# Performance work log

Measured on AMD Instinct MI355X. Metric: run time of the kernel, lower is better.

The kernel has to match this reference:

```python
import jax, jax.numpy as jnp
import numpy as np

N = 100000   # nodes
E = 600000   # edges
V = 64       # vocab
D = 128      # emb_dim
H = 128      # hidden_dim
G = 256      # graphs in batch


def setup_inputs():
    key = jax.random.key(0)
    ks = jax.random.split(key, 12)
    x_idx = jax.random.randint(ks[0], (N,), 0, V)
    edge_index = jax.random.randint(ks[1], (2, E), 0, N)
    batch = jnp.sort(jax.random.randint(ks[2], (N,), 0, G))
    emb = jax.random.normal(ks[3], (V, D), jnp.float32) * 0.02
    emb = emb.at[0].set(0.0)  # padding_idx=0
    def lin(k, o, i):
        return jax.random.normal(k, (o, i), jnp.float32) * (1.0 / np.sqrt(i))
    return dict(
        x_idx=x_idx, edge_index=edge_index, batch=batch, emb=emb,
        ln0_g=jnp.ones((D,), jnp.float32), ln0_b=jnp.zeros((D,), jnp.float32),
        w0_l=lin(ks[4], H, D), b0_l=jnp.zeros((H,), jnp.float32), w0_r=lin(ks[5], H, D),
        ln1_g=jnp.ones((H,), jnp.float32), ln1_b=jnp.zeros((H,), jnp.float32),
        w1_l=lin(ks[6], H, H), b1_l=jnp.zeros((H,), jnp.float32), w1_r=lin(ks[7], H, H),
        mlp_w1=lin(ks[8], H // 2, H), mlp_b1=jnp.zeros((H // 2,), jnp.float32),
        mlp_w2=lin(ks[9], 2, H // 2), mlp_b2=jnp.zeros((2,), jnp.float32),
    )


def _layernorm(x, g, b, eps=1e-5):
    m = jnp.mean(x, axis=-1, keepdims=True)
    v = jnp.var(x, axis=-1, keepdims=True)
    return (x - m) * jax.lax.rsqrt(v + eps) * g + b


def _sage_conv(x, src, dst, w_l, b_l, w_r):
    # PyG SAGEConv (mean aggr): out = lin_l(mean_{j->i} x_j) + lin_r(x_i)
    agg = jax.ops.segment_sum(x[src], dst, num_segments=N)        # [N, F]
    deg = jax.ops.segment_sum(jnp.ones((src.shape[0],), x.dtype), dst, num_segments=N)
    agg = agg / jnp.maximum(deg, 1.0)[:, None]
    return agg @ w_l.T + b_l + x @ w_r.T


def reference(x_idx, edge_index, batch, emb,
              ln0_g, ln0_b, w0_l, b0_l, w0_r,
              ln1_g, ln1_b, w1_l, b1_l, w1_r,
              mlp_w1, mlp_b1, mlp_w2, mlp_b2):
    src, dst = edge_index[0], edge_index[1]
    x = emb[x_idx]                                   # [N, D]
    # layer 0 (dropout is identity in eval mode)
    x = _layernorm(x, ln0_g, ln0_b)
    x = jax.nn.relu(_sage_conv(x, src, dst, w0_l, b0_l, w0_r))
    # layer 1
    x = _layernorm(x, ln1_g, ln1_b)
    x = jax.nn.relu(_sage_conv(x, src, dst, w1_l, b1_l, w1_r))
    # global mean pool over graphs
    sums = jax.ops.segment_sum(x, batch, num_segments=G)          # [G, H]
    cnts = jax.ops.segment_sum(jnp.ones((N,), x.dtype), batch, num_segments=G)
    g = sums / jnp.maximum(cnts, 1.0)[:, None]
    # MLP head
    h = jax.nn.relu(g @ mlp_w1.T + mlp_b1)
    return h @ mlp_w2.T + mlp_b2                                   # [G, 2]
```

## Files before the change

kernel.cpp:

```cpp
#include <hip/hip_runtime.h>

#define NN 100000
#define NE 600000
#define DIM 128
#define NG 256
#define NGRP 6250
#define NB_SCAN 391

typedef __attribute__((ext_vector_type(8))) short short8_t;
typedef __attribute__((ext_vector_type(4))) float f32x4;

__device__ __forceinline__ ushort f2bf(float f) {
  unsigned u = __float_as_uint(f);
  unsigned r = (u + 0x7fffu + ((u >> 16) & 1u)) >> 16;
  return (ushort)r;
}
__device__ __forceinline__ float bf2f(ushort h) {
  return __uint_as_float(((unsigned)h) << 16);
}

__global__ __launch_bounds__(256) void embed_ln_kernel(
    const int* __restrict__ x_idx, const float* __restrict__ emb,
    const float* __restrict__ g, const float* __restrict__ b,
    float* __restrict__ out) {
  int wave = threadIdx.x >> 6;
  int lane = threadIdx.x & 63;
  int n = blockIdx.x * 4 + wave;
  if (n >= NN) return;
  int idx = x_idx[n];
  float2 v = ((const float2*)(emb + (size_t)idx * DIM))[lane];
  float s = v.x + v.y;
  float sq = v.x * v.x + v.y * v.y;
  for (int off = 32; off; off >>= 1) {
    s += __shfl_xor(s, off);
    sq += __shfl_xor(sq, off);
  }
  float m = s * (1.0f / 128.0f);
  float var = sq * (1.0f / 128.0f) - m * m;
  float r = rsqrtf(var + 1e-5f);
  float2 gg = ((const float2*)g)[lane];
  float2 bb = ((const float2*)b)[lane];
  float2 o;
  o.x = (v.x - m) * r * gg.x + bb.x;
  o.y = (v.y - m) * r * gg.y + bb.y;
  ((float2*)(out + (size_t)n * DIM))[lane] = o;
}

__global__ __launch_bounds__(256) void deg_int_kernel(const int* __restrict__ dst,
                                                      int* __restrict__ degi) {
  int e = blockIdx.x * 256 + threadIdx.x;
  if (e < NE) atomicAdd(degi + dst[e], 1);
}

__global__ __launch_bounds__(256) void scan1_kernel(const int* __restrict__ degi,
                                                    int* __restrict__ excl,
                                                    int* __restrict__ bsum) {
  __shared__ int tmp[256];
  int t = threadIdx.x;
  int i = blockIdx.x * 256 + t;
  int v = (i < NN) ? degi[i] : 0;
  int val = v;
  tmp[t] = val;
  __syncthreads();
  for (int off = 1; off < 256; off <<= 1) {
    int add = (t >= off) ? tmp[t - off] : 0;
    __syncthreads();
    val += add;
    tmp[t] = val;
    __syncthreads();
  }
  if (i < NN) excl[i] = val - v;
  if (t == 255) bsum[blockIdx.x] = val;
}

__global__ __launch_bounds__(512) void scan2_kernel(int* __restrict__ bsum,
                                                    int* __restrict__ bscan) {
  __shared__ int tmp[512];
  int t = threadIdx.x;
  int v = (t < NB_SCAN) ? bsum[t] : 0;
  int val = v;
  tmp[t] = val;
  __syncthreads();
  for (int off = 1; off < 512; off <<= 1) {
    int add = (t >= off) ? tmp[t - off] : 0;
    __syncthreads();
    val += add;
    tmp[t] = val;
    __syncthreads();
  }
  if (t < NB_SCAN) bscan[t] = val - v;
}

__global__ __launch_bounds__(256) void scan3_kernel(const int* __restrict__ excl,
                                                    const int* __restrict__ bscan,
                                                    int* __restrict__ row_off,
                                                    int* __restrict__ cursor) {
  int i = blockIdx.x * 256 + threadIdx.x;
  if (i < NN) {
    int r = excl[i] + bscan[i >> 8];
    row_off[i] = r;
    cursor[i] = r;
  }
  if (i == 0) row_off[NN] = NE;
}

__global__ __launch_bounds__(256) void fill_kernel(const int* __restrict__ src,
                                                   const int* __restrict__ dst,
                                                   int* __restrict__ cursor,
                                                   int* __restrict__ csr_src) {
  int e = blockIdx.x * 256 + threadIdx.x;
  if (e < NE) {
    int d = dst[e];
    int slot = atomicAdd(cursor + d, 1);
    csr_src[slot] = src[e];
  }
}

__global__ __launch_bounds__(256) void gather_mean_kernel(
    const int* __restrict__ row_off, const int* __restrict__ csr_src,
    const float* __restrict__ x, ushort* __restrict__ af) {
  int t = threadIdx.x;
  int q = t & 31;
  int node = blockIdx.x * 8 + (t >> 5);
  if (node >= NN) return;
  int beg = row_off[node], end = row_off[node + 1];
  float4 acc = make_float4(0.f, 0.f, 0.f, 0.f);
  for (int e = beg; e < end; ++e) {
    int s = csr_src[e];
    float4 v = ((const float4*)(x + (size_t)s * DIM))[q];
    acc.x += v.x; acc.y += v.y; acc.z += v.z; acc.w += v.w;
  }
  float sc = 1.0f / fmaxf((float)(end - beg), 1.0f);
  acc.x *= sc; acc.y *= sc; acc.z *= sc; acc.w *= sc;
  ushort4 hi, lo;
  hi.x = f2bf(acc.x); lo.x = f2bf(acc.x - bf2f(hi.x));
  hi.y = f2bf(acc.y); lo.y = f2bf(acc.y - bf2f(hi.y));
  hi.z = f2bf(acc.z); lo.z = f2bf(acc.z - bf2f(hi.z));
  hi.w = f2bf(acc.w); lo.w = f2bf(acc.w - bf2f(hi.w));
  int g = node >> 4, l15n = node & 15;
  int jb = q >> 3, lqw = q & 3, ebase = q & 4;
  size_t base = (((size_t)g * 4 + jb) * 64 + lqw * 16 + l15n) * 16;
  *(ushort4*)(af + base + ebase) = hi;
  *(ushort4*)(af + base + 8 + ebase) = lo;
}

__global__ __launch_bounds__(256) void prep_w_kernel(const float* __restrict__ wl,
                                                     const float* __restrict__ wr,
                                                     ushort* __restrict__ wp) {
  int t = blockIdx.x * 256 + threadIdx.x;
  int e = t & 7;
  int lane = (t >> 3) & 63;
  int ht = (t >> 9) & 7;
  int j = (t >> 12) & 1;
  int p = (t >> 13) & 3;
  int h = ht * 16 + (lane & 15);
  int lq = lane >> 4;
  int k = p * 64 + j * 32 + lq * 4 + (e & 3) + 16 * (e >> 2);
  float v = (k < 128) ? wl[h * 128 + k] : wr[h * 128 + (k - 128)];
  ushort hi = f2bf(v);
  ushort lo = f2bf(v - bf2f(hi));
  wp[(((p * 2 + 0) * 2 + j) * 8 + ht) * 512 + lane * 8 + e] = hi;
  wp[(((p * 2 + 1) * 2 + j) * 8 + ht) * 512 + lane * 8 + e] = lo;
}

__global__ __launch_bounds__(256, 3) void conv_mfma_kernel(
    const float* __restrict__ xln, const ushort* __restrict__ af,
    const ushort* __restrict__ wp, const float* __restrict__ bl,
    const float* __restrict__ lng, const float* __restrict__ lnb,
    float* __restrict__ out, int do_ln) {
  __shared__ ushort Xs[2][128 * 64];
  const int t = threadIdx.x;
  const int lane = t & 63;
  const int wv = t >> 6;
  const int l15 = lane & 15;
  const int lq = lane >> 4;
  const int nbase = blockIdx.x * 128;

  f32x4 acc[2][8];
#pragma unroll
  for (int a = 0; a < 2; ++a)
#pragma unroll
    for (int b = 0; b < 8; ++b) acc[a][b] = (f32x4){0.f, 0.f, 0.f, 0.f};

  const int srow = t >> 1;
  const int sh2 = t & 1;
  const int gn_s = nbase + srow;
  const bool sval = gn_s < NN;
  char* lds_hi = (char*)&Xs[0][0];
  char* lds_lo = (char*)&Xs[1][0];
  const int sswz = (srow & 7) << 4;

#pragma unroll 1
  for (int ph = 0; ph < 2; ++ph) {
    if (ph) __syncthreads();
    const int kb = ph * 64;
#pragma unroll
    for (int i = 0; i < 8; ++i) {
      int qd = sh2 * 8 + i;
      float4 v = make_float4(0.f, 0.f, 0.f, 0.f);
      if (sval) v = *(const float4*)(xln + (size_t)gn_s * DIM + kb + qd * 4);
      int j = qd >> 3;
      int a = qd & 7;
      int inner = j * 64 + ((a < 4) ? a * 16 : (a - 4) * 16 + 8);
      int off = srow * 128 + inner;
      ushort4 hi, lo;
      hi.x = f2bf(v.x); lo.x = f2bf(v.x - bf2f(hi.x));
      hi.y = f2bf(v.y); lo.y = f2bf(v.y - bf2f(hi.y));
      hi.z = f2bf(v.z); lo.z = f2bf(v.z - bf2f(hi.z));
      hi.w = f2bf(v.w); lo.w = f2bf(v.w - bf2f(hi.w));
      *(ushort4*)(lds_hi + (off ^ sswz)) = hi;
      *(ushort4*)(lds_lo + (off ^ sswz)) = lo;
    }
    __syncthreads();
    const int pk = ph + 2;
#pragma unroll
    for (int j = 0; j < 2; ++j) {
      short8_t ahi[2], alo[2];
#pragma unroll
      for (int nt = 0; nt < 2; ++nt) {
        int row = wv * 32 + nt * 16 + l15;
        int off = row * 128 + j * 64 + lq * 16;
        int sw = (row & 7) << 4;
        ahi[nt] = *(short8_t*)(lds_hi + (off ^ sw));
        alo[nt] = *(short8_t*)(lds_lo + (off ^ sw));
      }
#pragma unroll
      for (int ht = 0; ht < 8; ++ht) {
        short8_t bhi = *(const short8_t*)(wp + (((pk * 2 + 0) * 2 + j) * 8 + ht) * 512 + lane * 8);
        short8_t blo = *(const short8_t*)(wp + (((pk * 2 + 1) * 2 + j) * 8 + ht) * 512 + lane * 8);
        acc[0][ht] = __builtin_amdgcn_mfma_f32_16x16x32_bf16(ahi[0], bhi, acc[0][ht], 0, 0, 0);
        acc[1][ht] = __builtin_amdgcn_mfma_f32_16x16x32_bf16(ahi[1], bhi, acc[1][ht], 0, 0, 0);
        acc[0][ht] = __builtin_amdgcn_mfma_f32_16x16x32_bf16(alo[0], bhi, acc[0][ht], 0, 0, 0);
        acc[1][ht] = __builtin_amdgcn_mfma_f32_16x16x32_bf16(alo[1], bhi, acc[1][ht], 0, 0, 0);
        acc[0][ht] = __builtin_amdgcn_mfma_f32_16x16x32_bf16(ahi[0], blo, acc[0][ht], 0, 0, 0);
        acc[1][ht] = __builtin_amdgcn_mfma_f32_16x16x32_bf16(ahi[1], blo, acc[1][ht], 0, 0, 0);
      }
    }
  }

  const int gblk = blockIdx.x * 8 + wv * 2;
#pragma unroll 1
  for (int ph = 2; ph < 4; ++ph) {
    const int pk = ph - 2;
#pragma unroll
    for (int j = 0; j < 2; ++j) {
      int jb = (ph & 1) * 2 + j;
      short8_t ahi[2], alo[2];
#pragma unroll
      for (int nt = 0; nt < 2; ++nt) {
        int g = gblk + nt;
        if (g < NGRP) {
          size_t base = (((size_t)g * 4 + jb) * 64 + lane) * 16;
          ahi[nt] = *(const short8_t*)(af + base);
          alo[nt] = *(const short8_t*)(af + base + 8);
        } else {
          ahi[nt] = (short8_t){0, 0, 0, 0, 0, 0, 0, 0};
          alo[nt] = (short8_t){0, 0, 0, 0, 0, 0, 0, 0};
        }
      }
#pragma unroll
      for (int ht = 0; ht < 8; ++ht) {
        short8_t bhi = *(const short8_t*)(wp + (((pk * 2 + 0) * 2 + j) * 8 + ht) * 512 + lane * 8);
        short8_t blo = *(const short8_t*)(wp + (((pk * 2 + 1) * 2 + j) * 8 + ht) * 512 + lane * 8);
        acc[0][ht] = __builtin_amdgcn_mfma_f32_16x16x32_bf16(ahi[0], bhi, acc[0][ht], 0, 0, 0);
        acc[1][ht] = __builtin_amdgcn_mfma_f32_16x16x32_bf16(ahi[1], bhi, acc[1][ht], 0, 0, 0);
        acc[0][ht] = __builtin_amdgcn_mfma_f32_16x16x32_bf16(alo[0], bhi, acc[0][ht], 0, 0, 0);
        acc[1][ht] = __builtin_amdgcn_mfma_f32_16x16x32_bf16(alo[1], bhi, acc[1][ht], 0, 0, 0);
        acc[0][ht] = __builtin_amdgcn_mfma_f32_16x16x32_bf16(ahi[0], blo, acc[0][ht], 0, 0, 0);
        acc[1][ht] = __builtin_amdgcn_mfma_f32_16x16x32_bf16(ahi[1], blo, acc[1][ht], 0, 0, 0);
      }
    }
  }

#pragma unroll
  for (int ht = 0; ht < 8; ++ht) {
    float bv = bl[ht * 16 + l15];
#pragma unroll
    for (int nt = 0; nt < 2; ++nt)
#pragma unroll
      for (int r = 0; r < 4; ++r) acc[nt][ht][r] = fmaxf(acc[nt][ht][r] + bv, 0.f);
  }
  if (do_ln) {
    float gg[8], bb[8];
#pragma unroll
    for (int ht = 0; ht < 8; ++ht) {
      gg[ht] = lng[ht * 16 + l15];
      bb[ht] = lnb[ht * 16 + l15];
    }
#pragma unroll
    for (int nt = 0; nt < 2; ++nt) {
#pragma unroll
      for (int r = 0; r < 4; ++r) {
        float s = 0.f, sq = 0.f;
#pragma unroll
        for (int ht = 0; ht < 8; ++ht) {
          float v = acc[nt][ht][r];
          s += v;
          sq += v * v;
        }
#pragma unroll
        for (int msk = 1; msk < 16; msk <<= 1) {
          s += __shfl_xor(s, msk);
          sq += __shfl_xor(sq, msk);
        }
        float m = s * (1.0f / 128.0f);
        float var = sq * (1.0f / 128.0f) - m * m;
        float rstd = rsqrtf(var + 1e-5f);
        int node = nbase + wv * 32 + nt * 16 + lq * 4 + r;
        if (node < NN) {
#pragma unroll
          for (int ht = 0; ht < 8; ++ht)
            out[(size_t)node * DIM + ht * 16 + l15] =
                (acc[nt][ht][r] - m) * rstd * gg[ht] + bb[ht];
        }
      }
    }
  } else {
#pragma unroll
    for (int nt = 0; nt < 2; ++nt) {
#pragma unroll
      for (int r = 0; r < 4; ++r) {
        int node = nbase + wv * 32 + nt * 16 + lq * 4 + r;
        if (node < NN) {
#pragma unroll
          for (int ht = 0; ht < 8; ++ht)
            out[(size_t)node * DIM + ht * 16 + l15] = acc[nt][ht][r];
        }
      }
    }
  }
}

#define PCHUNK 128
__global__ __launch_bounds__(128) void pool_kernel(const float* __restrict__ x,
                                                   const int* __restrict__ batch,
                                                   float* __restrict__ pool,
                                                   float* __restrict__ cnt) {
  int f = threadIdx.x;
  int n0 = blockIdx.x * PCHUNK;
  float acc = 0.f;
  int cur = batch[n0];
  int runlen = 0;
  for (int i = 0; i < PCHUNK; ++i) {
    int n = n0 + i;
    if (n >= NN) break;
    int bg = batch[n];
    if (bg != cur) {
      atomicAdd(&pool[cur * DIM + f], acc);
      if (f == 0) atomicAdd(&cnt[cur], (float)runlen);
      acc = 0.f;
      runlen = 0;
      cur = bg;
    }
    acc += x[(size_t)n * DIM + f];
    runlen++;
  }
  if (runlen > 0) {
    atomicAdd(&pool[cur * DIM + f], acc);
    if (f == 0) atomicAdd(&cnt[cur], (float)runlen);
  }
}

__global__ __launch_bounds__(128) void head_kernel(
    const float* __restrict__ pool, const float* __restrict__ cnt,
    const float* __restrict__ w1, const float* __restrict__ b1,
    const float* __restrict__ w2, const float* __restrict__ b2,
    float* __restrict__ out) {
  __shared__ float gsh[128];
  __shared__ float h[64];
  int g = blockIdx.x;
  int t = threadIdx.x;
  float ic = 1.0f / fmaxf(cnt[g], 1.0f);
  gsh[t] = pool[g * DIM + t] * ic;
  __syncthreads();
  if (t < 64) {
    float a = b1[t];
#pragma unroll 8
    for (int k = 0; k < 128; ++k) a += gsh[k] * w1[t * 128 + k];
    h[t] = fmaxf(a, 0.f);
  }
  __syncthreads();
  if (t < 2) {
    float a = b2[t];
#pragma unroll
    for (int k = 0; k < 64; ++k) a += h[k] * w2[t * 64 + k];
    out[g * 2 + t] = a;
  }
}

extern "C" void kernel_launch(void* const* d_in, const int* in_sizes, int n_in,
                              void* d_out, int out_size, void* d_ws, size_t ws_size,
                              hipStream_t stream) {
  const int* x_idx = (const int*)d_in[0];
  const int* eidx = (const int*)d_in[1];
  const int* batch = (const int*)d_in[2];
  const float* emb = (const float*)d_in[3];
  const float* ln0g = (const float*)d_in[4];
  const float* ln0b = (const float*)d_in[5];
  const float* w0l = (const float*)d_in[6];
  const float* b0l = (const float*)d_in[7];
  const float* w0r = (const float*)d_in[8];
  const float* ln1g = (const float*)d_in[9];
  const float* ln1b = (const float*)d_in[10];
  const float* w1l = (const float*)d_in[11];
  const float* b1l = (const float*)d_in[12];
  const float* w1r = (const float*)d_in[13];
  const float* mw1 = (const float*)d_in[14];
  const float* mb1 = (const float*)d_in[15];
  const float* mw2 = (const float*)d_in[16];
  const float* mb2 = (const float*)d_in[17];
  float* out = (float*)d_out;

  float* ws = (float*)d_ws;
  float* x = ws;
  ushort* af = (ushort*)(x + (size_t)NN * DIM);
  float* pool = (float*)(af + (size_t)NN * DIM * 2);
  float* cnt = pool + (size_t)NG * DIM;
  ushort* wp0 = (ushort*)(cnt + NG);
  ushort* wp1 = wp0 + 65536;
  int* degi = (int*)(wp1 + 65536);
  int* excl = degi + NN;
  int* row_off = excl + NN;
  int* cursor = row_off + NN + 1;
  int* bsum = cursor + NN;
  int* bscan = bsum + 512;
  int* csr_src = bscan + 512;

  const int* src = eidx;
  const int* dst = eidx + NE;

  hipMemsetAsync(pool, 0, ((size_t)NG * DIM + NG) * sizeof(float), stream);
  hipMemsetAsync(degi, 0, (size_t)NN * sizeof(int), stream);

  deg_int_kernel<<<(NE + 255) / 256, 256, 0, stream>>>(dst, degi);
  scan1_kernel<<<NB_SCAN, 256, 0, stream>>>(degi, excl, bsum);
  scan2_kernel<<<1, 512, 0, stream>>>(bsum, bscan);
  scan3_kernel<<<NB_SCAN, 256, 0, stream>>>(excl, bscan, row_off, cursor);
  fill_kernel<<<(NE + 255) / 256, 256, 0, stream>>>(src, dst, cursor, csr_src);

  prep_w_kernel<<<128, 256, 0, stream>>>(w0l, w0r, wp0);
  prep_w_kernel<<<128, 256, 0, stream>>>(w1l, w1r, wp1);

  embed_ln_kernel<<<NN / 4, 256, 0, stream>>>(x_idx, emb, ln0g, ln0b, x);

  gather_mean_kernel<<<(NN + 7) / 8, 256, 0, stream>>>(row_off, csr_src, x, af);
  conv_mfma_kernel<<<(NN + 127) / 128, 256, 0, stream>>>(x, af, wp0, b0l, ln1g, ln1b, x, 1);
  gather_mean_kernel<<<(NN + 7) / 8, 256, 0, stream>>>(row_off, csr_src, x, af);
  conv_mfma_kernel<<<(NN + 127) / 128, 256, 0, stream>>>(x, af, wp1, b1l, (const float*)0, (const float*)0, x, 0);

  pool_kernel<<<(NN + PCHUNK - 1) / PCHUNK, 128, 0, stream>>>(x, batch, pool, cnt);
  head_kernel<<<NG, 128, 0, stream>>>(pool, cnt, mw1, mb1, mw2, mb2, out);
}
```

Baseline: 461.0 us.

## Fuse neighbor gather-mean into SAGE MFMA kernel and merge setup kernels

The neighbor mean aggregation now runs inside the conv kernel. It writes split-bf16 operands straight into LDS instead of round-tripping a global af buffer, and ping-pongs between x and y buffers. The root-feature half now loads fp32 rows directly into registers and splits them there, with no LDS staging. The scan2/scan3 pair becomes one kernel that has each block reduce prior block sums. CSR fill, weight prep and the embedding layernorm merge into one launch, and the two memsets become one. This cuts launches and global traffic. The cost is a serial gather phase before the MFMA work in each block, plus lower occupancy (launch bounds go from 3 to 2) with a larger LDS tile.

```diff
diff --git a/kernel.cpp b/kernel.cpp
--- a/kernel.cpp
+++ b/kernel.cpp
@@ -4,8 +4,10 @@
 #define NE 600000
 #define DIM 128
 #define NG 256
-#define NGRP 6250
 #define NB_SCAN 391
+#define FILL_NB 2344
+#define PREP_NB 128
+#define EMB_NB 25000
 
 typedef __attribute__((ext_vector_type(8))) short short8_t;
 typedef __attribute__((ext_vector_type(4))) float f32x4;
@@ -17,33 +19,6 @@
 }
 __device__ __forceinline__ float bf2f(ushort h) {
   return __uint_as_float(((unsigned)h) << 16);
-}
-
-__global__ __launch_bounds__(256) void embed_ln_kernel(
-    const int* __restrict__ x_idx, const float* __restrict__ emb,
-    const float* __restrict__ g, const float* __restrict__ b,
-    float* __restrict__ out) {
-  int wave = threadIdx.x >> 6;
-  int lane = threadIdx.x & 63;
-  int n = blockIdx.x * 4 + wave;
-  if (n >= NN) return;
-  int idx = x_idx[n];
-  float2 v = ((const float2*)(emb + (size_t)idx * DIM))[lane];
-  float s = v.x + v.y;
-  float sq = v.x * v.x + v.y * v.y;
-  for (int off = 32; off; off >>= 1) {
-    s += __shfl_xor(s, off);
-    sq += __shfl_xor(sq, off);
-  }
-  float m = s * (1.0f / 128.0f);
-  float var = sq * (1.0f / 128.0f) - m * m;
-  float r = rsqrtf(var + 1e-5f);
-  float2 gg = ((const float2*)g)[lane];
-  float2 bb = ((const float2*)b)[lane];
-  float2 o;
-  o.x = (v.x - m) * r * gg.x + bb.x;
-  o.y = (v.y - m) * r * gg.y + bb.y;
-  ((float2*)(out + (size_t)n * DIM))[lane] = o;
 }
 
 __global__ __launch_bounds__(256) void deg_int_kernel(const int* __restrict__ dst,
@@ -73,42 +48,36 @@
   if (t == 255) bsum[blockIdx.x] = val;
 }
 
-__global__ __launch_bounds__(512) void scan2_kernel(int* __restrict__ bsum,
-                                                    int* __restrict__ bscan) {
-  __shared__ int tmp[512];
+__global__ __launch_bounds__(256) void scan23_kernel(const int* __restrict__ excl,
+                                                     const int* __restrict__ bsum,
+                                                     int* __restrict__ row_off,
+                                                     int* __restrict__ cursor) {
+  __shared__ int sh[256];
+  int blk = blockIdx.x;
   int t = threadIdx.x;
-  int v = (t < NB_SCAN) ? bsum[t] : 0;
-  int val = v;
-  tmp[t] = val;
+  int partial = 0;
+  for (int j = t; j < blk; j += 256) partial += bsum[j];
+  sh[t] = partial;
   __syncthreads();
-  for (int off = 1; off < 512; off <<= 1) {
-    int add = (t >= off) ? tmp[t - off] : 0;
+  for (int off = 128; off; off >>= 1) {
+    if (t < off) sh[t] += sh[t + off];
     __syncthreads();
-    val += add;
-    tmp[t] = val;
-    __syncthreads();
-  }
-  if (t < NB_SCAN) bscan[t] = val - v;
-}
-
-__global__ __launch_bounds__(256) void scan3_kernel(const int* __restrict__ excl,
-                                                    const int* __restrict__ bscan,
-                                                    int* __restrict__ row_off,
-                                                    int* __restrict__ cursor) {
-  int i = blockIdx.x * 256 + threadIdx.x;
+  }
+  int base = sh[0];
+  int i = blk * 256 + t;
   if (i < NN) {
-    int r = excl[i] + bscan[i >> 8];
+    int r = excl[i] + base;
     row_off[i] = r;
     cursor[i] = r;
   }
-  if (i == 0) row_off[NN] = NE;
-}
-
-__global__ __launch_bounds__(256) void fill_kernel(const int* __restrict__ src,
-                                                   const int* __restrict__ dst,
-                                                   int* __restrict__ cursor,
-                                                   int* __restrict__ csr_src) {
-  int e = blockIdx.x * 256 + threadIdx.x;
+  if (i == NN) row_off[NN] = NE;
+}
+
+__device__ __forceinline__ void fill_body(int bid, int t, const int* __restrict__ src,
+                                          const int* __restrict__ dst,
+                                          int* __restrict__ cursor,
+                                          int* __restrict__ csr_src) {
+  int e = bid * 256 + t;
   if (e < NE) {
     int d = dst[e];
     int slot = atomicAdd(cursor + d, 1);
@@ -116,43 +85,14 @@
   }
 }
 
-__global__ __launch_bounds__(256) void gather_mean_kernel(
-    const int* __restrict__ row_off, const int* __restrict__ csr_src,
-    const float* __restrict__ x, ushort* __restrict__ af) {
-  int t = threadIdx.x;
-  int q = t & 31;
-  int node = blockIdx.x * 8 + (t >> 5);
-  if (node >= NN) return;
-  int beg = row_off[node], end = row_off[node + 1];
-  float4 acc = make_float4(0.f, 0.f, 0.f, 0.f);
-  for (int e = beg; e < end; ++e) {
-    int s = csr_src[e];
-    float4 v = ((const float4*)(x + (size_t)s * DIM))[q];
-    acc.x += v.x; acc.y += v.y; acc.z += v.z; acc.w += v.w;
-  }
-  float sc = 1.0f / fmaxf((float)(end - beg), 1.0f);
-  acc.x *= sc; acc.y *= sc; acc.z *= sc; acc.w *= sc;
-  ushort4 hi, lo;
-  hi.x = f2bf(acc.x); lo.x = f2bf(acc.x - bf2f(hi.x));
-  hi.y = f2bf(acc.y); lo.y = f2bf(acc.y - bf2f(hi.y));
-  hi.z = f2bf(acc.z); lo.z = f2bf(acc.z - bf2f(hi.z));
-  hi.w = f2bf(acc.w); lo.w = f2bf(acc.w - bf2f(hi.w));
-  int g = node >> 4, l15n = node & 15;
-  int jb = q >> 3, lqw = q & 3, ebase = q & 4;
-  size_t base = (((size_t)g * 4 + jb) * 64 + lqw * 16 + l15n) * 16;
-  *(ushort4*)(af + base + ebase) = hi;
-  *(ushort4*)(af + base + 8 + ebase) = lo;
-}
-
-__global__ __launch_bounds__(256) void prep_w_kernel(const float* __restrict__ wl,
-                                                     const float* __restrict__ wr,
-                                                     ushort* __restrict__ wp) {
-  int t = blockIdx.x * 256 + threadIdx.x;
-  int e = t & 7;
-  int lane = (t >> 3) & 63;
-  int ht = (t >> 9) & 7;
-  int j = (t >> 12) & 1;
-  int p = (t >> 13) & 3;
+__device__ __forceinline__ void prep_body(int idx, const float* __restrict__ wl,
+                                          const float* __restrict__ wr,
+                                          ushort* __restrict__ wp) {
+  int e = idx & 7;
+  int lane = (idx >> 3) & 63;
+  int ht = (idx >> 9) & 7;
+  int j = (idx >> 12) & 1;
+  int p = (idx >> 13) & 3;
   int h = ht * 16 + (lane & 15);
   int lq = lane >> 4;
   int k = p * 64 + j * 32 + lq * 4 + (e & 3) + 16 * (e >> 2);
@@ -163,12 +103,61 @@
   wp[(((p * 2 + 1) * 2 + j) * 8 + ht) * 512 + lane * 8 + e] = lo;
 }
 
-__global__ __launch_bounds__(256, 3) void conv_mfma_kernel(
-    const float* __restrict__ xln, const ushort* __restrict__ af,
-    const ushort* __restrict__ wp, const float* __restrict__ bl,
-    const float* __restrict__ lng, const float* __restrict__ lnb,
-    float* __restrict__ out, int do_ln) {
-  __shared__ ushort Xs[2][128 * 64];
+__device__ __forceinline__ void embed_body(int bid, int t, const int* __restrict__ x_idx,
+                                           const float* __restrict__ emb,
+                                           const float* __restrict__ g,
+                                           const float* __restrict__ b,
+                                           float* __restrict__ out) {
+  int wave = t >> 6;
+  int lane = t & 63;
+  int n = bid * 4 + wave;
+  if (n >= NN) return;
+  int idx = x_idx[n];
+  float2 v = ((const float2*)(emb + (size_t)idx * DIM))[lane];
+  float s = v.x + v.y;
+  float sq = v.x * v.x + v.y * v.y;
+  for (int off = 32; off; off >>= 1) {
+    s += __shfl_xor(s, off);
+    sq += __shfl_xor(sq, off);
+  }
+  float m = s * (1.0f / 128.0f);
+  float var = sq * (1.0f / 128.0f) - m * m;
+  float r = rsqrtf(var + 1e-5f);
+  float2 gg = ((const float2*)g)[lane];
+  float2 bb = ((const float2*)b)[lane];
+  float2 o;
+  o.x = (v.x - m) * r * gg.x + bb.x;
+  o.y = (v.y - m) * r * gg.y + bb.y;
+  ((float2*)(out + (size_t)n * DIM))[lane] = o;
+}
+
+__global__ __launch_bounds__(256) void mega_kernel(
+    const int* __restrict__ src, const int* __restrict__ dst,
+    int* __restrict__ cursor, int* __restrict__ csr_src,
+    const float* __restrict__ w0l, const float* __restrict__ w0r, ushort* __restrict__ wp0,
+    const float* __restrict__ w1l, const float* __restrict__ w1r, ushort* __restrict__ wp1,
+    const int* __restrict__ x_idx, const float* __restrict__ emb,
+    const float* __restrict__ ln0g, const float* __restrict__ ln0b,
+    float* __restrict__ x) {
+  int bid = blockIdx.x;
+  int t = threadIdx.x;
+  if (bid < FILL_NB) {
+    fill_body(bid, t, src, dst, cursor, csr_src);
+  } else if (bid < FILL_NB + PREP_NB) {
+    prep_body((bid - FILL_NB) * 256 + t, w0l, w0r, wp0);
+  } else if (bid < FILL_NB + 2 * PREP_NB) {
+    prep_body((bid - FILL_NB - PREP_NB) * 256 + t, w1l, w1r, wp1);
+  } else {
+    embed_body(bid - FILL_NB - 2 * PREP_NB, t, x_idx, emb, ln0g, ln0b, x);
+  }
+}
+
+__global__ __launch_bounds__(256, 2) void sage_kernel(
+    const float* __restrict__ xin, const int* __restrict__ row_off,
+    const int* __restrict__ csr_src, const ushort* __restrict__ wp,
+    const float* __restrict__ bl, const float* __restrict__ lng,
+    const float* __restrict__ lnb, float* __restrict__ out, int do_ln) {
+  __shared__ ushort Aagg[8 * 4 * 2 * 64 * 8];
   const int t = threadIdx.x;
   const int lane = t & 63;
   const int wv = t >> 6;
@@ -176,99 +165,106 @@
   const int lq = lane >> 4;
   const int nbase = blockIdx.x * 128;
 
+  {
+    const int q = t & 31;
+    const int nr = t >> 5;
+    const int jb = q >> 3, lqw = q & 3, ebase = q & 4;
+#pragma unroll 1
+    for (int r = 0; r < 16; ++r) {
+      int nl = r * 8 + nr;
+      int node = nbase + nl;
+      float4 a4 = make_float4(0.f, 0.f, 0.f, 0.f);
+      int beg = 0, end = 0;
+      if (node < NN) { beg = row_off[node]; end = row_off[node + 1]; }
+      int e = beg;
+      int s = (e < end) ? csr_src[e] : 0;
+      while (e < end) {
+        int snx = (e + 1 < end) ? csr_src[e + 1] : 0;
+        float4 v = ((const float4*)(xin + (size_t)s * DIM))[q];
+        a4.x += v.x; a4.y += v.y; a4.z += v.z; a4.w += v.w;
+        s = snx;
+        ++e;
+      }
+      float sc = 1.0f / fmaxf((float)(end - beg), 1.0f);
+      a4.x *= sc; a4.y *= sc; a4.z *= sc; a4.w *= sc;
+      ushort4 hi, lo;
+      hi.x = f2bf(a4.x); lo.x = f2bf(a4.x - bf2f(hi.x));
+      hi.y = f2bf(a4.y); lo.y = f2bf(a4.y - bf2f(hi.y));
+      hi.z = f2bf(a4.z); lo.z = f2bf(a4.z - bf2f(hi.z));
+      hi.w = f2bf(a4.w); lo.w = f2bf(a4.w - bf2f(hi.w));
+      int g = nl >> 4, l15n = nl & 15;
+      int bh = (((g * 4 + jb) * 2 + 0) * 64 + lqw * 16 + l15n) * 8;
+      *(ushort4*)(Aagg + bh + ebase) = hi;
+      *(ushort4*)(Aagg + bh + 512 + ebase) = lo;
+    }
+  }
+  __syncthreads();
+
   f32x4 acc[2][8];
 #pragma unroll
   for (int a = 0; a < 2; ++a)
 #pragma unroll
     for (int b = 0; b < 8; ++b) acc[a][b] = (f32x4){0.f, 0.f, 0.f, 0.f};
 
-  const int srow = t >> 1;
-  const int sh2 = t & 1;
-  const int gn_s = nbase + srow;
-  const bool sval = gn_s < NN;
-  char* lds_hi = (char*)&Xs[0][0];
-  char* lds_lo = (char*)&Xs[1][0];
-  const int sswz = (srow & 7) << 4;
-
-#pragma unroll 1
-  for (int ph = 0; ph < 2; ++ph) {
-    if (ph) __syncthreads();
-    const int kb = ph * 64;
-#pragma unroll
-    for (int i = 0; i < 8; ++i) {
-      int qd = sh2 * 8 + i;
-      float4 v = make_float4(0.f, 0.f, 0.f, 0.f);
-      if (sval) v = *(const float4*)(xln + (size_t)gn_s * DIM + kb + qd * 4);
-      int j = qd >> 3;
-      int a = qd & 7;
-      int inner = j * 64 + ((a < 4) ? a * 16 : (a - 4) * 16 + 8);
-      int off = srow * 128 + inner;
-      ushort4 hi, lo;
-      hi.x = f2bf(v.x); lo.x = f2bf(v.x - bf2f(hi.x));
-      hi.y = f2bf(v.y); lo.y = f2bf(v.y - bf2f(hi.y));
-      hi.z = f2bf(v.z); lo.z = f2bf(v.z - bf2f(hi.z));
-      hi.w = f2bf(v.w); lo.w = f2bf(v.w - bf2f(hi.w));
-      *(ushort4*)(lds_hi + (off ^ sswz)) = hi;
-      *(ushort4*)(lds_lo + (off ^ sswz)) = lo;
-    }
-    __syncthreads();
-    const int pk = ph + 2;
-#pragma unroll
-    for (int j = 0; j < 2; ++j) {
-      short8_t ahi[2], alo[2];
-#pragma unroll
-      for (int nt = 0; nt < 2; ++nt) {
-        int row = wv * 32 + nt * 16 + l15;
-        int off = row * 128 + j * 64 + lq * 16;
-        int sw = (row & 7) << 4;
-        ahi[nt] = *(short8_t*)(lds_hi + (off ^ sw));
-        alo[nt] = *(short8_t*)(lds_lo + (off ^ sw));
+#pragma unroll
+  for (int jb = 0; jb < 4; ++jb) {
+    const int pk = jb >> 1, j = jb & 1;
+    short8_t ahi[2], alo[2];
+#pragma unroll
+    for (int nt = 0; nt < 2; ++nt) {
+      int gl = wv * 2 + nt;
+      int ba = (((gl * 4 + jb) * 2 + 0) * 64 + lane) * 8;
+      ahi[nt] = *(const short8_t*)(Aagg + ba);
+      alo[nt] = *(const short8_t*)(Aagg + ba + 512);
+    }
+#pragma unroll
+    for (int ht = 0; ht < 8; ++ht) {
+      short8_t bhi = *(const short8_t*)(wp + (((pk * 2 + 0) * 2 + j) * 8 + ht) * 512 + lane * 8);
+      short8_t blo = *(const short8_t*)(wp + (((pk * 2 + 1) * 2 + j) * 8 + ht) * 512 + lane * 8);
+      acc[0][ht] = __builtin_amdgcn_mfma_f32_16x16x32_bf16(ahi[0], bhi, acc[0][ht], 0, 0, 0);
+      acc[1][ht] = __builtin_amdgcn_mfma_f32_16x16x32_bf16(ahi[1], bhi, acc[1][ht], 0, 0, 0);
+      acc[0][ht] = __builtin_amdgcn_mfma_f32_16x16x32_bf16(alo[0], bhi, acc[0][ht], 0, 0, 0);
+      acc[1][ht] = __builtin_amdgcn_mfma_f32_16x16x32_bf16(alo[1], bhi, acc[1][ht], 0, 0, 0);
+      acc[0][ht] = __builtin_amdgcn_mfma_f32_16x16x32_bf16(ahi[0], blo, acc[0][ht], 0, 0, 0);
+      acc[1][ht] = __builtin_amdgcn_mfma_f32_16x16x32_bf16(ahi[1], blo, acc[1][ht], 0, 0, 0);
+    }
+  }
+
+#pragma unroll
+  for (int pks = 0; pks < 4; ++pks) {
+    const int pk = 2 + (pks >> 1), j = pks & 1;
+    short8_t ahi[2], alo[2];
+#pragma unroll
+    for (int nt = 0; nt < 2; ++nt) {
+      int node = nbase + wv * 32 + nt * 16 + l15;
+      float4 fa = make_float4(0.f, 0.f, 0.f, 0.f);
+      float4 fb = make_float4(0.f, 0.f, 0.f, 0.f);
+      if (node < NN) {
+        const float* rp = xin + (size_t)node * DIM + pks * 32 + lq * 4;
+        fa = *(const float4*)rp;
+        fb = *(const float4*)(rp + 16);
       }
-#pragma unroll
-      for (int ht = 0; ht < 8; ++ht) {
-        short8_t bhi = *(const short8_t*)(wp + (((pk * 2 + 0) * 2 + j) * 8 + ht) * 512 + lane * 8);
-        short8_t blo = *(const short8_t*)(wp + (((pk * 2 + 1) * 2 + j) * 8 + ht) * 512 + lane * 8);
-        acc[0][ht] = __builtin_amdgcn_mfma_f32_16x16x32_bf16(ahi[0], bhi, acc[0][ht], 0, 0, 0);
-        acc[1][ht] = __builtin_amdgcn_mfma_f32_16x16x32_bf16(ahi[1], bhi, acc[1][ht], 0, 0, 0);
-        acc[0][ht] = __builtin_amdgcn_mfma_f32_16x16x32_bf16(alo[0], bhi, acc[0][ht], 0, 0, 0);
-        acc[1][ht] = __builtin_amdgcn_mfma_f32_16x16x32_bf16(alo[1], bhi, acc[1][ht], 0, 0, 0);
-        acc[0][ht] = __builtin_amdgcn_mfma_f32_16x16x32_bf16(ahi[0], blo, acc[0][ht], 0, 0, 0);
-        acc[1][ht] = __builtin_amdgcn_mfma_f32_16x16x32_bf16(ahi[1], blo, acc[1][ht], 0, 0, 0);
+      float f[8] = {fa.x, fa.y, fa.z, fa.w, fb.x, fb.y, fb.z, fb.w};
+      short8_t h, l;
+#pragma unroll
+      for (int e = 0; e < 8; ++e) {
+        ushort hh = f2bf(f[e]);
+        h[e] = (short)hh;
+        l[e] = (short)f2bf(f[e] - bf2f(hh));
       }
-    }
-  }
-
-  const int gblk = blockIdx.x * 8 + wv * 2;
-#pragma unroll 1
-  for (int ph = 2; ph < 4; ++ph) {
-    const int pk = ph - 2;
-#pragma unroll
-    for (int j = 0; j < 2; ++j) {
-      int jb = (ph & 1) * 2 + j;
-      short8_t ahi[2], alo[2];
-#pragma unroll
-      for (int nt = 0; nt < 2; ++nt) {
-        int g = gblk + nt;
-        if (g < NGRP) {
-          size_t base = (((size_t)g * 4 + jb) * 64 + lane) * 16;
-          ahi[nt] = *(const short8_t*)(af + base);
-          alo[nt] = *(const short8_t*)(af + base + 8);
-        } else {
-          ahi[nt] = (short8_t){0, 0, 0, 0, 0, 0, 0, 0};
-          alo[nt] = (short8_t){0, 0, 0, 0, 0, 0, 0, 0};
-        }
-      }
-#pragma unroll
-      for (int ht = 0; ht < 8; ++ht) {
-        short8_t bhi = *(const short8_t*)(wp + (((pk * 2 + 0) * 2 + j) * 8 + ht) * 512 + lane * 8);
-        short8_t blo = *(const short8_t*)(wp + (((pk * 2 + 1) * 2 + j) * 8 + ht) * 512 + lane * 8);
-        acc[0][ht] = __builtin_amdgcn_mfma_f32_16x16x32_bf16(ahi[0], bhi, acc[0][ht], 0, 0, 0);
-        acc[1][ht] = __builtin_amdgcn_mfma_f32_16x16x32_bf16(ahi[1], bhi, acc[1][ht], 0, 0, 0);
-        acc[0][ht] = __builtin_amdgcn_mfma_f32_16x16x32_bf16(alo[0], bhi, acc[0][ht], 0, 0, 0);
-        acc[1][ht] = __builtin_amdgcn_mfma_f32_16x16x32_bf16(alo[1], bhi, acc[1][ht], 0, 0, 0);
-        acc[0][ht] = __builtin_amdgcn_mfma_f32_16x16x32_bf16(ahi[0], blo, acc[0][ht], 0, 0, 0);
-        acc[1][ht] = __builtin_amdgcn_mfma_f32_16x16x32_bf16(ahi[1], blo, acc[1][ht], 0, 0, 0);
-      }
+      ahi[nt] = h;
+      alo[nt] = l;
+    }
+#pragma unroll
+    for (int ht = 0; ht < 8; ++ht) {
+      short8_t bhi = *(const short8_t*)(wp + (((pk * 2 + 0) * 2 + j) * 8 + ht) * 512 + lane * 8);
+      short8_t blo = *(const short8_t*)(wp + (((pk * 2 + 1) * 2 + j) * 8 + ht) * 512 + lane * 8);
+      acc[0][ht] = __builtin_amdgcn_mfma_f32_16x16x32_bf16(ahi[0], bhi, acc[0][ht], 0, 0, 0);
+      acc[1][ht] = __builtin_amdgcn_mfma_f32_16x16x32_bf16(ahi[1], bhi, acc[1][ht], 0, 0, 0);
+      acc[0][ht] = __builtin_amdgcn_mfma_f32_16x16x32_bf16(alo[0], bhi, acc[0][ht], 0, 0, 0);
+      acc[1][ht] = __builtin_amdgcn_mfma_f32_16x16x32_bf16(alo[1], bhi, acc[1][ht], 0, 0, 0);
+      acc[0][ht] = __builtin_amdgcn_mfma_f32_16x16x32_bf16(ahi[0], blo, acc[0][ht], 0, 0, 0);
+      acc[1][ht] = __builtin_amdgcn_mfma_f32_16x16x32_bf16(ahi[1], blo, acc[1][ht], 0, 0, 0);
     }
   }
 
@@ -413,40 +409,33 @@
 
   float* ws = (float*)d_ws;
   float* x = ws;
-  ushort* af = (ushort*)(x + (size_t)NN * DIM);
-  float* pool = (float*)(af + (size_t)NN * DIM * 2);
+  float* y = x + (size_t)NN * DIM;
+  float* pool = y + (size_t)NN * DIM;
   float* cnt = pool + (size_t)NG * DIM;
-  ushort* wp0 = (ushort*)(cnt + NG);
-  ushort* wp1 = wp0 + 65536;
-  int* degi = (int*)(wp1 + 65536);
+  int* degi = (int*)(cnt + NG);
   int* excl = degi + NN;
   int* row_off = excl + NN;
   int* cursor = row_off + NN + 1;
   int* bsum = cursor + NN;
-  int* bscan = bsum + 512;
-  int* csr_src = bscan + 512;
+  int* csr_src = bsum + 512;
+  ushort* wp0 = (ushort*)(csr_src + NE);
+  ushort* wp1 = wp0 + 65536;
 
   const int* src = eidx;
   const int* dst = eidx + NE;
 
-  hipMemsetAsync(pool, 0, ((size_t)NG * DIM + NG) * sizeof(float), stream);
-  hipMemsetAsync(degi, 0, (size_t)NN * sizeof(int), stream);
-
-  deg_int_kernel<<<(NE + 255) / 256, 256, 0, stream>>>(dst, degi);
+  hipMemsetAsync(pool, 0, ((size_t)NG * DIM + NG + NN) * sizeof(float), stream);
+
+  deg_int_kernel<<<FILL_NB, 256, 0, stream>>>(dst, degi);
   scan1_kernel<<<NB_SCAN, 256, 0, stream>>>(degi, excl, bsum);
-  scan2_kernel<<<1, 512, 0, stream>>>(bsum, bscan);
-  scan3_kernel<<<NB_SCAN, 256, 0, stream>>>(excl, bscan, row_off, cursor);
-  fill_kernel<<<(NE + 255) / 256, 256, 0, stream>>>(src, dst, cursor, csr_src);
-
-  prep_w_kernel<<<128, 256, 0, stream>>>(w0l, w0r, wp0);
-  prep_w_kernel<<<128, 256, 0, stream>>>(w1l, w1r, wp1);
-
-  embed_ln_kernel<<<NN / 4, 256, 0, stream>>>(x_idx, emb, ln0g, ln0b, x);
-
-  gather_mean_kernel<<<(NN + 7) / 8, 256, 0, stream>>>(row_off, csr_src, x, af);
-  conv_mfma_kernel<<<(NN + 127) / 128, 256, 0, stream>>>(x, af, wp0, b0l, ln1g, ln1b, x, 1);
-  gather_mean_kernel<<<(NN + 7) / 8, 256, 0, stream>>>(row_off, csr_src, x, af);
-  conv_mfma_kernel<<<(NN + 127) / 128, 256, 0, stream>>>(x, af, wp1, b1l, (const float*)0, (const float*)0, x, 0);
+  scan23_kernel<<<NB_SCAN, 256, 0, stream>>>(excl, bsum, row_off, cursor);
+  mega_kernel<<<FILL_NB + 2 * PREP_NB + EMB_NB, 256, 0, stream>>>(
+      src, dst, cursor, csr_src, w0l, w0r, wp0, w1l, w1r, wp1, x_idx, emb, ln0g, ln0b, x);
+
+  sage_kernel<<<(NN + 127) / 128, 256, 0, stream>>>(x, row_off, csr_src, wp0, b0l,
+                                                    ln1g, ln1b, y, 1);
+  sage_kernel<<<(NN + 127) / 128, 256, 0, stream>>>(y, row_off, csr_src, wp1, b1l,
+                                                    (const float*)0, (const float*)0, x, 0);
 
   pool_kernel<<<(NN + PCHUNK - 1) / PCHUNK, 128, 0, stream>>>(x, batch, pool, cnt);
   head_kernel<<<NG, 128, 0, stream>>>(pool, cnt, mw1, mb1, mw2, mb2, out);
```

Measured after the change: 577.8 us. 1.25x slower.

## Merge scan passes, fuse setup kernels into one launch, merge memsets

Applied to the files above, without the earlier changes.

Folds scan2 and scan3 into one kernel in which each block reduces the preceding block sums itself. The CSR fill, both weight-prep passes and the embedding layernorm now run in a single block-partitioned mega kernel, and the two memsets become one by reordering the workspace so degi follows the pool buffers. conv_mfma launch bounds also rise from 3 to 5 blocks per CU. The aim is to cut launch count and let independent setup work overlap, at the cost of redundant bsum reads in the scan and possible register spills in conv.

```diff
diff --git a/kernel.cpp b/kernel.cpp
--- a/kernel.cpp
+++ b/kernel.cpp
@@ -6,6 +6,9 @@
 #define NG 256
 #define NGRP 6250
 #define NB_SCAN 391
+#define FILL_NB 2344
+#define PREP_NB 128
+#define EMB_NB 25000
 
 typedef __attribute__((ext_vector_type(8))) short short8_t;
 typedef __attribute__((ext_vector_type(4))) float f32x4;
@@ -17,33 +20,6 @@
 }
 __device__ __forceinline__ float bf2f(ushort h) {
   return __uint_as_float(((unsigned)h) << 16);
-}
-
-__global__ __launch_bounds__(256) void embed_ln_kernel(
-    const int* __restrict__ x_idx, const float* __restrict__ emb,
-    const float* __restrict__ g, const float* __restrict__ b,
-    float* __restrict__ out) {
-  int wave = threadIdx.x >> 6;
-  int lane = threadIdx.x & 63;
-  int n = blockIdx.x * 4 + wave;
-  if (n >= NN) return;
-  int idx = x_idx[n];
-  float2 v = ((const float2*)(emb + (size_t)idx * DIM))[lane];
-  float s = v.x + v.y;
-  float sq = v.x * v.x + v.y * v.y;
-  for (int off = 32; off; off >>= 1) {
-    s += __shfl_xor(s, off);
-    sq += __shfl_xor(sq, off);
-  }
-  float m = s * (1.0f / 128.0f);
-  float var = sq * (1.0f / 128.0f) - m * m;
-  float r = rsqrtf(var + 1e-5f);
-  float2 gg = ((const float2*)g)[lane];
-  float2 bb = ((const float2*)b)[lane];
-  float2 o;
-  o.x = (v.x - m) * r * gg.x + bb.x;
-  o.y = (v.y - m) * r * gg.y + bb.y;
-  ((float2*)(out + (size_t)n * DIM))[lane] = o;
 }
 
 __global__ __launch_bounds__(256) void deg_int_kernel(const int* __restrict__ dst,
@@ -73,46 +49,107 @@
   if (t == 255) bsum[blockIdx.x] = val;
 }
 
-__global__ __launch_bounds__(512) void scan2_kernel(int* __restrict__ bsum,
-                                                    int* __restrict__ bscan) {
-  __shared__ int tmp[512];
+__global__ __launch_bounds__(256) void scan23_kernel(const int* __restrict__ excl,
+                                                     const int* __restrict__ bsum,
+                                                     int* __restrict__ row_off,
+                                                     int* __restrict__ cursor) {
+  __shared__ int sh[256];
+  int blk = blockIdx.x;
   int t = threadIdx.x;
-  int v = (t < NB_SCAN) ? bsum[t] : 0;
-  int val = v;
-  tmp[t] = val;
+  int partial = 0;
+  for (int j = t; j < blk; j += 256) partial += bsum[j];
+  sh[t] = partial;
   __syncthreads();
-  for (int off = 1; off < 512; off <<= 1) {
-    int add = (t >= off) ? tmp[t - off] : 0;
+  for (int off = 128; off; off >>= 1) {
+    if (t < off) sh[t] += sh[t + off];
     __syncthreads();
-    val += add;
-    tmp[t] = val;
-    __syncthreads();
-  }
-  if (t < NB_SCAN) bscan[t] = val - v;
-}
-
-__global__ __launch_bounds__(256) void scan3_kernel(const int* __restrict__ excl,
-                                                    const int* __restrict__ bscan,
-                                                    int* __restrict__ row_off,
-                                                    int* __restrict__ cursor) {
-  int i = blockIdx.x * 256 + threadIdx.x;
+  }
+  int base = sh[0];
+  int i = blk * 256 + t;
   if (i < NN) {
-    int r = excl[i] + bscan[i >> 8];
+    int r = excl[i] + base;
     row_off[i] = r;
     cursor[i] = r;
   }
-  if (i == 0) row_off[NN] = NE;
-}
-
-__global__ __launch_bounds__(256) void fill_kernel(const int* __restrict__ src,
-                                                   const int* __restrict__ dst,
-                                                   int* __restrict__ cursor,
-                                                   int* __restrict__ csr_src) {
-  int e = blockIdx.x * 256 + threadIdx.x;
+  if (i == NN) row_off[NN] = NE;
+}
+
+__device__ __forceinline__ void fill_body(int bid, int t, const int* __restrict__ src,
+                                          const int* __restrict__ dst,
+                                          int* __restrict__ cursor,
+                                          int* __restrict__ csr_src) {
+  int e = bid * 256 + t;
   if (e < NE) {
     int d = dst[e];
     int slot = atomicAdd(cursor + d, 1);
     csr_src[slot] = src[e];
+  }
+}
+
+__device__ __forceinline__ void prep_body(int idx, const float* __restrict__ wl,
+                                          const float* __restrict__ wr,
+                                          ushort* __restrict__ wp) {
+  int e = idx & 7;
+  int lane = (idx >> 3) & 63;
+  int ht = (idx >> 9) & 7;
+  int j = (idx >> 12) & 1;
+  int p = (idx >> 13) & 3;
+  int h = ht * 16 + (lane & 15);
+  int lq = lane >> 4;
+  int k = p * 64 + j * 32 + lq * 4 + (e & 3) + 16 * (e >> 2);
+  float v = (k < 128) ? wl[h * 128 + k] : wr[h * 128 + (k - 128)];
+  ushort hi = f2bf(v);
+  ushort lo = f2bf(v - bf2f(hi));
+  wp[(((p * 2 + 0) * 2 + j) * 8 + ht) * 512 + lane * 8 + e] = hi;
+  wp[(((p * 2 + 1) * 2 + j) * 8 + ht) * 512 + lane * 8 + e] = lo;
+}
+
+__device__ __forceinline__ void embed_body(int bid, int t, const int* __restrict__ x_idx,
+                                           const float* __restrict__ emb,
+                                           const float* __restrict__ g,
+                                           const float* __restrict__ b,
+                                           float* __restrict__ out) {
+  int wave = t >> 6;
+  int lane = t & 63;
+  int n = bid * 4 + wave;
+  if (n >= NN) return;
+  int idx = x_idx[n];
+  float2 v = ((const float2*)(emb + (size_t)idx * DIM))[lane];
+  float s = v.x + v.y;
+  float sq = v.x * v.x + v.y * v.y;
+  for (int off = 32; off; off >>= 1) {
+    s += __shfl_xor(s, off);
+    sq += __shfl_xor(sq, off);
+  }
+  float m = s * (1.0f / 128.0f);
+  float var = sq * (1.0f / 128.0f) - m * m;
+  float r = rsqrtf(var + 1e-5f);
+  float2 gg = ((const float2*)g)[lane];
+  float2 bb = ((const float2*)b)[lane];
+  float2 o;
+  o.x = (v.x - m) * r * gg.x + bb.x;
+  o.y = (v.y - m) * r * gg.y + bb.y;
+  ((float2*)(out + (size_t)n * DIM))[lane] = o;
+}
+
+__global__ __launch_bounds__(256) void mega_kernel(
+    const int* __restrict__ src, const int* __restrict__ dst,
+    int* __restrict__ cursor, int* __restrict__ csr_src,
+    const float* __restrict__ w0l, const float* __restrict__ w0r, ushort* __restrict__ wp0,
+    const float* __restrict__ w1l, const float* __restrict__ w1r, ushort* __restrict__ wp1,
+    const int* __restrict__ x_idx, const float* __restrict__ emb,
+    const float* __restrict__ ln0g, const float* __restrict__ ln0b,
+    float* __restrict__ x) {
+  int bid = blockIdx.x;
+  int t = threadIdx.x;
+  if (bid < FILL_NB) {
+    fill_body(bid, t, src, dst, cursor, csr_src);
+  } else if (bid < FILL_NB + PREP_NB) {
+    prep_body((bid - FILL_NB) * 256 + t, w0l, w0r, wp0);
+  } else if (bid < FILL_NB + 2 * PREP_NB) {
+    prep_body((bid - FILL_NB - PREP_NB) * 256 + t, w1l, w1r, wp1);
+  } else {
+    embed_body(bid - FILL_NB - 2 * PREP_NB, t, x_idx, emb, ln0g, ln0b, x);
   }
 }
 
@@ -144,26 +181,7 @@
   *(ushort4*)(af + base + 8 + ebase) = lo;
 }
 
-__global__ __launch_bounds__(256) void prep_w_kernel(const float* __restrict__ wl,
-                                                     const float* __restrict__ wr,
-                                                     ushort* __restrict__ wp) {
-  int t = blockIdx.x * 256 + threadIdx.x;
-  int e = t & 7;
-  int lane = (t >> 3) & 63;
-  int ht = (t >> 9) & 7;
-  int j = (t >> 12) & 1;
-  int p = (t >> 13) & 3;
-  int h = ht * 16 + (lane & 15);
-  int lq = lane >> 4;
-  int k = p * 64 + j * 32 + lq * 4 + (e & 3) + 16 * (e >> 2);
-  float v = (k < 128) ? wl[h * 128 + k] : wr[h * 128 + (k - 128)];
-  ushort hi = f2bf(v);
-  ushort lo = f2bf(v - bf2f(hi));
-  wp[(((p * 2 + 0) * 2 + j) * 8 + ht) * 512 + lane * 8 + e] = hi;
-  wp[(((p * 2 + 1) * 2 + j) * 8 + ht) * 512 + lane * 8 + e] = lo;
-}
-
-__global__ __launch_bounds__(256, 3) void conv_mfma_kernel(
+__global__ __launch_bounds__(256, 5) void conv_mfma_kernel(
     const float* __restrict__ xln, const ushort* __restrict__ af,
     const ushort* __restrict__ wp, const float* __restrict__ bl,
     const float* __restrict__ lng, const float* __restrict__ lnb,
@@ -416,32 +434,25 @@
   ushort* af = (ushort*)(x + (size_t)NN * DIM);
   float* pool = (float*)(af + (size_t)NN * DIM * 2);
   float* cnt = pool + (size_t)NG * DIM;
-  ushort* wp0 = (ushort*)(cnt + NG);
-  ushort* wp1 = wp0 + 65536;
-  int* degi = (int*)(wp1 + 65536);
+  int* degi = (int*)(cnt + NG);
   int* excl = degi + NN;
   int* row_off = excl + NN;
   int* cursor = row_off + NN + 1;
   int* bsum = cursor + NN;
-  int* bscan = bsum + 512;
-  int* csr_src = bscan + 512;
+  int* csr_src = bsum + 512;
+  ushort* wp0 = (ushort*)(csr_src + NE);
+  ushort* wp1 = wp0 + 65536;
 
   const int* src = eidx;
   const int* dst = eidx + NE;
 
-  hipMemsetAsync(pool, 0, ((size_t)NG * DIM + NG) * sizeof(float), stream);
-  hipMemsetAsync(degi, 0, (size_t)NN * sizeof(int), stream);
-
-  deg_int_kernel<<<(NE + 255) / 256, 256, 0, stream>>>(dst, degi);
+  hipMemsetAsync(pool, 0, ((size_t)NG * DIM + NG + NN) * sizeof(float), stream);
+
+  deg_int_kernel<<<FILL_NB, 256, 0, stream>>>(dst, degi);
   scan1_kernel<<<NB_SCAN, 256, 0, stream>>>(degi, excl, bsum);
-  scan2_kernel<<<1, 512, 0, stream>>>(bsum, bscan);
-  scan3_kernel<<<NB_SCAN, 256, 0, stream>>>(excl, bscan, row_off, cursor);
-  fill_kernel<<<(NE + 255) / 256, 256, 0, stream>>>(src, dst, cursor, csr_src);
-
-  prep_w_kernel<<<128, 256, 0, stream>>>(w0l, w0r, wp0);
-  prep_w_kernel<<<128, 256, 0, stream>>>(w1l, w1r, wp1);
-
-  embed_ln_kernel<<<NN / 4, 256, 0, stream>>>(x_idx, emb, ln0g, ln0b, x);
+  scan23_kernel<<<NB_SCAN, 256, 0, stream>>>(excl, bsum, row_off, cursor);
+  mega_kernel<<<FILL_NB + 2 * PREP_NB + EMB_NB, 256, 0, stream>>>(
+      src, dst, cursor, csr_src, w0l, w0r, wp0, w1l, w1r, wp1, x_idx, emb, ln0g, ln0b, x);
 
   gather_mean_kernel<<<(NN + 7) / 8, 256, 0, stream>>>(row_off, csr_src, x, af);
   conv_mfma_kernel<<<(NN + 127) / 128, 256, 0, stream>>>(x, af, wp0, b0l, ln1g, ln1b, x, 1);
```

Result: slower. 547.8 us (+18.8%).
